# Kernel optimization log

Hardware: AMD Instinct MI355X
Metric: run time of the kernel (lower is better)

Reference implementation:

```python
import jax, jax.numpy as jnp
import numpy as np

B, S, E = 2, 4096, 640
H, D, G = 4, 256, 1      # n_heads, head_dim, n_kv_groups
WINDOW = 512
SCALING = 256.0 ** -0.5  # query_pre_attn_scalar ** -0.5
EPS = 1e-6


def rmsnorm(x, scale):
    # Gemma variant: weight = 1 + scale, computed in fp32 over last dim
    xf = x.astype(jnp.float32)
    var = jnp.mean(xf * xf, axis=-1, keepdims=True)
    return (xf * jax.lax.rsqrt(var + EPS) * (1.0 + scale.astype(jnp.float32))).astype(x.dtype)


def apply_rope(x, cos, sin):
    # x: [B, h, S, D]; cos/sin: [S, D]
    half = x.shape[-1] // 2
    x1, x2 = x[..., :half], x[..., half:]
    rotated = jnp.concatenate([-x2, x1], axis=-1)
    return (x * cos[None, None] + rotated * sin[None, None]).astype(x.dtype)


def setup_inputs() -> dict:
    key = jax.random.key(0)
    ks = jax.random.split(key, 6)
    x = jax.random.normal(ks[0], (B, S, E), dtype=jnp.float32)
    # weights (torch Linear weight.T layout: [in, out])
    Wq = jax.random.normal(ks[1], (E, H * D), dtype=jnp.float32) * 0.02
    Wk = jax.random.normal(ks[2], (E, G * D), dtype=jnp.float32) * 0.02
    Wv = jax.random.normal(ks[3], (E, G * D), dtype=jnp.float32) * 0.02
    Wo = jax.random.normal(ks[4], (H * D, E), dtype=jnp.float32) * 0.02
    q_scale = jnp.zeros((D,), dtype=jnp.float32)
    k_scale = jnp.zeros((D,), dtype=jnp.float32)
    # RoPE tables (theta = rope_local_base = 10000 for sliding layers)
    inv_freq = 1.0 / (10000.0 ** (jnp.arange(0, D, 2, dtype=jnp.float32) / D))
    angles = jnp.arange(S, dtype=jnp.float32)[:, None] * inv_freq[None, :]
    angles = jnp.concatenate([angles, angles], axis=1)  # [S, D]
    cos, sin = jnp.cos(angles), jnp.sin(angles)
    # causal + sliding-window mask; True = masked out
    i = jnp.arange(S)[:, None]
    j = jnp.arange(S)[None, :]
    mask = (j > i) | ((i - j) >= WINDOW)
    return {"x": x, "mask": mask, "cos": cos, "sin": sin,
            "Wq": Wq, "Wk": Wk, "Wv": Wv, "Wo": Wo,
            "q_scale": q_scale, "k_scale": k_scale}


def reference(x, mask, cos, sin, Wq, Wk, Wv, Wo, q_scale, k_scale):
    b, s, _ = x.shape
    q = (x @ Wq).reshape(b, s, H, D).transpose(0, 2, 1, 3)  # [B,H,S,D]
    k = (x @ Wk).reshape(b, s, G, D).transpose(0, 2, 1, 3)  # [B,G,S,D]
    v = (x @ Wv).reshape(b, s, G, D).transpose(0, 2, 1, 3)  # [B,G,S,D]
    q = rmsnorm(q, q_scale)
    k = rmsnorm(k, k_scale)
    q = apply_rope(q, cos, sin)
    k = apply_rope(k, cos, sin)
    # GQA: K/V have G=1 heads; broadcasting replaces repeat_interleave
    scores = (q * SCALING) @ jnp.swapaxes(k, -1, -2)  # [B,H,S,S]
    scores = jnp.where(mask[None, None], -jnp.inf, scores)
    attn = jax.nn.softmax(scores, axis=-1)
    out = attn @ v                                     # [B,H,S,D]
    out = out.transpose(0, 2, 1, 3).reshape(b, s, H * D)
    return out @ Wo
```

## Files before the change

kernel.cpp:

```cpp
#include <hip/hip_runtime.h>
#include <hip/hip_bf16.h>
#include <stdint.h>

#define BB 2
#define SS 4096
#define EE 640
#define HH 4
#define DD 256
#define WIN 512

typedef __attribute__((ext_vector_type(8))) short bv8;
typedef __attribute__((ext_vector_type(4))) float fv4;
typedef __attribute__((ext_vector_type(16))) float fv16;

__device__ __forceinline__ unsigned short f2b(float f) {
  union { float f; unsigned u; } a; a.f = f;
  unsigned r = a.u + 0x7fffu + ((a.u >> 16) & 1u);
  return (unsigned short)(r >> 16);
}
__device__ __forceinline__ float b2f(unsigned short s) {
  union { unsigned u; float f; } a; a.u = ((unsigned)s) << 16;
  return a.f;
}
__device__ __forceinline__ unsigned pk2(float lo, float hi_) {
  return (unsigned)f2b(lo) | ((unsigned)f2b(hi_) << 16);
}

typedef const __attribute__((address_space(1))) unsigned int* as1u;
typedef __attribute__((address_space(3))) unsigned int* as3u;
__device__ __forceinline__ void gld16(const unsigned short* g, unsigned short* l) {
  __builtin_amdgcn_global_load_lds((as1u)(const void*)g, (as3u)(void*)l, 16, 0, 0);
}

__global__ __launch_bounds__(256) void k_cast_bf16(const float* __restrict__ src,
                                                   unsigned short* __restrict__ dst, int n4) {
  int i = blockIdx.x * 256 + threadIdx.x;
  if (i >= n4) return;
  fv4 v = ((const fv4*)src)[i];
  ushort4 o; o.x = f2b(v.x); o.y = f2b(v.y); o.z = f2b(v.z); o.w = f2b(v.w);
  ((ushort4*)dst)[i] = o;
}

__global__ __launch_bounds__(256) void k_wtrans(const float* __restrict__ Wq,
    const float* __restrict__ Wk, const float* __restrict__ Wv,
    const float* __restrict__ Wo, const float* __restrict__ cosp,
    const float* __restrict__ sinp, unsigned short* __restrict__ wqkv,
    unsigned short* __restrict__ wo, float* __restrict__ ctab) {
  const int z = blockIdx.z, bx = blockIdx.x, by = blockIdx.y;
  const int t = threadIdx.x;
  if (z == 4) {
    const int bb = bx * 32 + by;
    const int s = bb * 4 + (t >> 6);
#pragma unroll
    for (int k = 0; k < 4; ++k) {
      int c = (t & 63) * 4 + k;
      int lr = c >> 4, wn2 = (c >> 3) & 1, j = c & 7;
      int d = wn2 * 64 + (j & 3) * 16 + lr;
      float v = (j < 4) ? cosp[(size_t)s * 256 + d] : sinp[(size_t)s * 256 + d];
      ctab[(size_t)s * 256 + c] = v;
    }
    return;
  }
  __shared__ float tile[32][33];
  const float* src; unsigned short* dst; int ss, ds;
  if (z == 0)      { if (bx >= 20 || by >= 32) return; src = Wq; dst = wqkv;              ss = 1024; ds = 640; }
  else if (z == 1) { if (bx >= 20 || by >= 8)  return; src = Wk; dst = wqkv + 1024 * 640; ss = 256;  ds = 640; }
  else if (z == 2) { if (bx >= 20 || by >= 8)  return; src = Wv; dst = wqkv + 1280 * 640; ss = 256;  ds = 640; }
  else             { if (bx >= 32 || by >= 20) return; src = Wo; dst = wo;                ss = 640;  ds = 1024; }
  int r0 = bx * 32, c0 = by * 32;
  int rr = t >> 3, cc = (t & 7) * 4;
  fv4 x = *(const fv4*)(src + (size_t)(r0 + rr) * ss + c0 + cc);
#pragma unroll
  for (int i = 0; i < 4; ++i) tile[cc + i][rr] = x[i];
  __syncthreads();
  ushort4 o;
  o.x = f2b(tile[rr][cc + 0]); o.y = f2b(tile[rr][cc + 1]);
  o.z = f2b(tile[rr][cc + 2]); o.w = f2b(tile[rr][cc + 3]);
  *(ushort4*)(dst + (size_t)(c0 + rr) * ds + r0 + cc) = o;
}

__global__ __launch_bounds__(256) void k_gemm_qkv(const unsigned short* __restrict__ A,
    const unsigned short* __restrict__ Bt, const float* __restrict__ ctab,
    const float* __restrict__ qsc, const float* __restrict__ ksc,
    unsigned short* __restrict__ qo, unsigned short* __restrict__ ko,
    unsigned short* __restrict__ vt) {
  __shared__ __align__(16) char shl[40960];
  unsigned short* la = (unsigned short*)shl;
  unsigned short* lb = (unsigned short*)(shl + 8192);
  const int K = EE;
  const int bid = blockIdx.x;
  const int gidx = (bid & 7) * 96 + (bid >> 3);
  const int mt = gidx / 6, nt = gidx % 6;
  const int m0 = mt * 64, n0 = nt * 256;
  const int tid = threadIdx.x, lane = tid & 63, wave = tid >> 6;
  const int g = lane >> 4, lr = lane & 15;
  const int wm = (wave >> 1) * 32, wn2 = wave & 1;
  fv4 acc[2][8] = {};
  const unsigned short* ga0 = A + (size_t)(m0 + (tid >> 2)) * K + (tid & 3) * 8;
  const unsigned short* gb0 = Bt + (size_t)(n0 + (tid >> 2)) * K + (tid & 3) * 8;
  auto stage = [&](int k0, int pp) {
    gld16(ga0 + k0, la + pp * 2048 + wave * 512);
#pragma unroll
    for (int c = 0; c < 4; ++c)
      gld16(gb0 + (size_t)(c * 64) * K + k0, lb + pp * 8192 + (c * 64 + wave * 16) * 32);
  };
  stage(0, 0);
  const int NIT = K >> 5;
  for (int it = 0; it < NIT; ++it) {
    const int p = it & 1;
    if (it > 0) __builtin_amdgcn_s_barrier();
    if (it + 1 < NIT) {
      stage((it + 1) * 32, p ^ 1);
      asm volatile("s_waitcnt vmcnt(5)" ::: "memory");
    } else {
      asm volatile("s_waitcnt vmcnt(0)" ::: "memory");
    }
    __builtin_amdgcn_sched_barrier(0);
    __builtin_amdgcn_s_barrier();
    bv8 af[2], bf[8];
#pragma unroll
    for (int mi = 0; mi < 2; ++mi)
      af[mi] = *(const bv8*)(la + p * 2048 + (wm + mi * 16 + lr) * 32 + g * 8);
#pragma unroll
    for (int ni = 0; ni < 8; ++ni) {
      int coln = wn2 * 64 + (ni & 3) * 16 + (ni >> 2) * 128 + lr;
      bf[ni] = *(const bv8*)(lb + p * 8192 + coln * 32 + g * 8);
    }
    __builtin_amdgcn_s_setprio(1);
#pragma unroll
    for (int mi = 0; mi < 2; ++mi)
#pragma unroll
      for (int ni = 0; ni < 8; ++ni)
        acc[mi][ni] = __builtin_amdgcn_mfma_f32_16x16x32_bf16(af[mi], bf[ni], acc[mi][ni], 0, 0, 0);
    __builtin_amdgcn_s_setprio(0);
  }
  __syncthreads();
  if (nt < 5) {
    float* rsum = (float*)(shl + 36864);
    float part[2][4];
#pragma unroll
    for (int mi = 0; mi < 2; ++mi)
#pragma unroll
      for (int r = 0; r < 4; ++r) {
        float ss2 = 0.f;
#pragma unroll
        for (int ni = 0; ni < 8; ++ni) ss2 += acc[mi][ni][r] * acc[mi][ni][r];
        part[mi][r] = ss2;
      }
#pragma unroll
    for (int off = 1; off < 16; off <<= 1)
#pragma unroll
      for (int mi = 0; mi < 2; ++mi)
#pragma unroll
        for (int r = 0; r < 4; ++r) part[mi][r] += __shfl_xor(part[mi][r], off, 64);
    if (lr == 0) {
#pragma unroll
      for (int mi = 0; mi < 2; ++mi)
#pragma unroll
        for (int r = 0; r < 4; ++r)
          rsum[(wm + mi * 16 + g * 4 + r) * 2 + wn2] = part[mi][r];
    }
    __syncthreads();
    const float* scp = (nt < 4) ? qsc : ksc;
    const float mult = (nt < 4) ? (0.0625f * 1.44269504f) : 1.0f;
    float scl[8];
#pragma unroll
    for (int ni = 0; ni < 8; ++ni) {
      int d = wn2 * 64 + (ni & 3) * 16 + (ni >> 2) * 128 + lr;
      scl[ni] = 1.0f + scp[d];
    }
#pragma unroll
    for (int mi = 0; mi < 2; ++mi)
#pragma unroll
      for (int r = 0; r < 4; ++r) {
        int row = wm + mi * 16 + g * 4 + r;
        int mabs = m0 + row;
        int bb = mabs >> 12, s = mabs & 4095;
        float tot = rsum[row * 2 + 0] + rsum[row * 2 + 1];
        float rs = rsqrtf(tot * (1.0f / 256.0f) + 1e-6f);
        fv4 c4 = *(const fv4*)(ctab + (size_t)s * 256 + lr * 16 + wn2 * 8);
        fv4 s4 = *(const fv4*)(ctab + (size_t)s * 256 + lr * 16 + wn2 * 8 + 4);
        unsigned short* dst = (nt < 4)
            ? qo + ((size_t)(bb * HH + nt) * SS + s) * 256
            : ko + ((size_t)bb * SS + s) * 256;
#pragma unroll
        for (int j = 0; j < 4; ++j) {
          float nlo = acc[mi][j][r] * rs * scl[j];
          float nhi = acc[mi][j + 4][r] * rs * scl[j + 4];
          float olo = (nlo * c4[j] - nhi * s4[j]) * mult;
          float ohi = (nhi * c4[j] + nlo * s4[j]) * mult;
          int dlo = wn2 * 64 + j * 16 + lr;
          dst[dlo] = f2b(olo);
          dst[dlo + 128] = f2b(ohi);
        }
      }
  } else {
    unsigned short* vcol = (unsigned short*)shl;
#pragma unroll
    for (int mi = 0; mi < 2; ++mi)
#pragma unroll
      for (int ni = 0; ni < 8; ++ni) {
        int col = wn2 * 64 + (ni & 3) * 16 + (ni >> 2) * 128 + lr;
        int row0 = wm + mi * 16 + g * 4;
        uint2 u;
        u.x = pk2(acc[mi][ni][0], acc[mi][ni][1]);
        u.y = pk2(acc[mi][ni][2], acc[mi][ni][3]);
        *(uint2*)(vcol + col * 72 + row0) = u;
      }
    __syncthreads();
    const int d = tid;
    const int bb0 = m0 >> 12, s0 = m0 & 4095;
    unsigned short* dst = vt + ((size_t)bb0 * 256 + d) * SS + s0;
#pragma unroll
    for (int c8 = 0; c8 < 8; ++c8) {
      bv8 v = *(const bv8*)(vcol + d * 72 + c8 * 8);
      *(bv8*)(dst + c8 * 8) = v;
    }
  }
}

template <bool OUT_BF16, int BN>
__global__ __launch_bounds__(256) void k_gemm(const unsigned short* __restrict__ A,
    const unsigned short* __restrict__ Bt, void* __restrict__ Cp,
    int M, int N, int K, int nt_n) {
  __shared__ unsigned short la[2][128 * 32];
  __shared__ unsigned short lb[2][BN * 32];
  const int bid = blockIdx.x;
  const int gidx = (bid & 7) * (gridDim.x >> 3) + (bid >> 3);
  const int m0 = (gidx / nt_n) * 128, n0 = (gidx % nt_n) * BN;
  const int tid = threadIdx.x, lane = tid & 63, wave = tid >> 6;
  const int g = lane >> 4, lr = lane & 15;
  constexpr int MI = (BN == 128) ? 4 : 2;
  const int wm = (BN == 128) ? (wave >> 1) * 64 : wave * 32;
  const int wn = (BN == 128) ? (wave & 1) * 64 : 0;
  fv4 acc[MI][4] = {};
  const int srow = wave * 32 + (lane >> 2);
  const int sch = (lane & 3) * 8;
  const unsigned short* ga0 = A + (size_t)(m0 + srow) * K + sch;
  const int srowb = (BN == 128) ? srow : (wave * 16 + (lane >> 2));
  const unsigned short* gb0 = Bt + (size_t)(n0 + srowb) * K + sch;
  const int NIT = K >> 5;
  auto stage = [&](int k0, int pp) {
    unsigned short* lad = la[pp] + wave * 1024;
    unsigned short* lbd = lb[pp] + ((BN == 128) ? wave * 1024 : wave * 512);
    gld16(ga0 + k0, lad);
    gld16(ga0 + (size_t)16 * K + k0, lad + 512);
    gld16(gb0 + k0, lbd);
    if constexpr (BN == 128) gld16(gb0 + (size_t)16 * K + k0, lbd + 512);
  };
  stage(0, 0);
  for (int it = 0; it < NIT; ++it) {
    const int p = it & 1;
    if (it > 0) __builtin_amdgcn_s_barrier();
    if (it + 1 < NIT) {
      stage((it + 1) * 32, p ^ 1);
      if constexpr (BN == 128)
        asm volatile("s_waitcnt vmcnt(4)" ::: "memory");
      else
        asm volatile("s_waitcnt vmcnt(3)" ::: "memory");
    } else {
      asm volatile("s_waitcnt vmcnt(0)" ::: "memory");
    }
    __builtin_amdgcn_sched_barrier(0);
    __builtin_amdgcn_s_barrier();
    bv8 af[MI], bf[4];
#pragma unroll
    for (int mi = 0; mi < MI; ++mi)
      af[mi] = *(const bv8*)(la[p] + (wm + mi * 16 + lr) * 32 + g * 8);
#pragma unroll
    for (int ni = 0; ni < 4; ++ni)
      bf[ni] = *(const bv8*)(lb[p] + (wn + ni * 16 + lr) * 32 + g * 8);
    __builtin_amdgcn_s_setprio(1);
#pragma unroll
    for (int mi = 0; mi < MI; ++mi)
#pragma unroll
      for (int ni = 0; ni < 4; ++ni)
        acc[mi][ni] = __builtin_amdgcn_mfma_f32_16x16x32_bf16(af[mi], bf[ni], acc[mi][ni], 0, 0, 0);
    __builtin_amdgcn_s_setprio(0);
  }
#pragma unroll
  for (int mi = 0; mi < MI; ++mi) {
#pragma unroll
    for (int r = 0; r < 4; ++r) {
      size_t row = (size_t)(m0 + wm + mi * 16 + g * 4 + r);
#pragma unroll
      for (int ni = 0; ni < 4; ++ni) {
        int col = n0 + wn + ni * 16 + lr;
        float val = acc[mi][ni][r];
        if constexpr (OUT_BF16)
          ((unsigned short*)Cp)[row * N + col] = f2b(val);
        else
          ((float*)Cp)[row * N + col] = val;
      }
    }
  }
}

__global__ __launch_bounds__(512, 2) void k_attn(const unsigned short* __restrict__ q,
    const unsigned short* __restrict__ kg, const unsigned short* __restrict__ vtg,
    unsigned short* __restrict__ att) {
  __shared__ __align__(16) char ldsbuf[133120];
  __shared__ float lsb[4][32];
  unsigned short* kt = (unsigned short*)ldsbuf;
  unsigned short* vl = (unsigned short*)ldsbuf + 32768;
  const int bid = blockIdx.x;
  const int gidx = (bid & 7) * 32 + (bid >> 3);
  const int b = gidx >> 7;
  const int i0 = (gidx & 127) * 32;
  const int tid = threadIdx.x, wave = tid >> 6, lane = tid & 63;
  const int h = wave >> 1, ks = wave & 1;
  const int hi = lane >> 5, l31 = lane & 31;
  bv8 qf[16];
  {
    const unsigned short* qp = q + ((size_t)(b * HH + h) * SS + i0 + l31) * 256;
#pragma unroll
    for (int m = 0; m < 16; ++m) qf[m] = *(const bv8*)(qp + m * 16 + hi * 8);
  }
  fv16 po[8] = {};
  float lsp = 0.f;
  const int t0 = (i0 >= WIN) ? ((i0 - WIN + 1) >> 6) : 0;
  const int t1 = i0 >> 6;
  const unsigned short* kb = kg + (size_t)b * SS * 256;
  const unsigned short* vb = vtg + (size_t)b * 256 * SS;
  auto stageK = [&](int t, int pp) {
    const unsigned short* kbase = kb + (size_t)t * 64 * 256;
    unsigned short* dst = kt + pp * 16384;
#pragma unroll
    for (int c = 0; c < 4; ++c) {
      int slot = c * 512 + tid;
      int row = slot >> 5, s = slot & 31;
      gld16(kbase + (size_t)row * 256 + ((s ^ (row & 7)) * 8),
            dst + (c * 512 + wave * 64) * 8);
    }
  };
  auto stageV = [&](int t, int pp) {
    const unsigned short* vbase = vb + (size_t)t * 64;
    unsigned short* dst = vl + pp * 16384;
#pragma unroll
    for (int c = 0; c < 4; ++c) {
      int slot = c * 512 + tid;
      int d_ = slot >> 3, s = slot & 7;
      gld16(vbase + (size_t)d_ * SS + ((s ^ (d_ & 7)) * 8),
            dst + (c * 512 + wave * 64) * 8);
    }
  };
  stageK(t0, 0); stageV(t0, 0);
  int p = 0;
  const int krow = ks * 32 + l31;
  const int krx = krow & 7;
  const int vrx = l31 & 7;
  const float FSUB = 16.5f * 1.44269504f;
  for (int t = t0; t <= t1; ++t) {
    __syncthreads();
    if (t < t1) { stageK(t + 1, p ^ 1); stageV(t + 1, p ^ 1); }
    fv16 sa = {};
    const unsigned short* ktp = kt + p * 16384 + krow * 256;
    __builtin_amdgcn_s_setprio(1);
#pragma unroll
    for (int m = 0; m < 16; ++m) {
      bv8 kf = *(const bv8*)(ktp + (((m * 2 + hi) ^ krx) * 8));
      sa = __builtin_amdgcn_mfma_f32_32x32x16_bf16(kf, qf[m], sa, 0, 0, 0);
    }
    __builtin_amdgcn_s_setprio(0);
    const int kb0 = t * 64 + ks * 32;
    const bool nm = (kb0 + 31 > i0) || (i0 + 31 - kb0 >= WIN);
    if (nm) {
      const int qa = i0 + l31;
#pragma unroll
      for (int r = 0; r < 16; ++r) {
        int j = kb0 + (r & 3) + 8 * (r >> 2) + 4 * hi;
        if (j > qa || qa - j >= WIN) sa[r] = -1e30f;
      }
    }
    unsigned a[8];
#pragma unroll
    for (int i = 0; i < 8; ++i) {
      float e0 = exp2f(sa[2 * i] - FSUB);
      float e1 = exp2f(sa[2 * i + 1] - FSUB);
      lsp += e0 + e1;
      a[i] = pk2(e0, e1);
    }
    const unsigned short* vlp = vl + p * 16384;
    __builtin_amdgcn_s_setprio(1);
#pragma unroll
    for (int m2 = 0; m2 < 2; ++m2) {
      auto r02 = __builtin_amdgcn_permlane32_swap(a[m2 * 4 + 0], a[m2 * 4 + 2], false, false);
      auto r13 = __builtin_amdgcn_permlane32_swap(a[m2 * 4 + 1], a[m2 * 4 + 3], false, false);
      union { unsigned u[4]; bv8 v; } pf;
      pf.u[0] = r02[0]; pf.u[1] = r13[0]; pf.u[2] = r02[1]; pf.u[3] = r13[1];
      const int slot = (ks * 4 + m2 * 2 + hi) ^ vrx;
#pragma unroll
      for (int ds_ = 0; ds_ < 8; ++ds_) {
        bv8 vf = *(const bv8*)(vlp + (ds_ * 32 + l31) * 64 + slot * 8);
        po[ds_] = __builtin_amdgcn_mfma_f32_32x32x16_bf16(vf, pf.v, po[ds_], 0, 0, 0);
      }
    }
    __builtin_amdgcn_s_setprio(0);
    p ^= 1;
  }
  float lsfull = lsp + __shfl_xor(lsp, 32, 64);
  __syncthreads();
  float* cb = (float*)ldsbuf;
  if (ks == 1) {
#pragma unroll
    for (int ds_ = 0; ds_ < 8; ++ds_)
#pragma unroll
      for (int j = 0; j < 4; ++j) {
        int d0 = ds_ * 32 + 8 * j + 4 * hi;
        fv4 v4; v4[0] = po[ds_][4 * j]; v4[1] = po[ds_][4 * j + 1];
        v4[2] = po[ds_][4 * j + 2]; v4[3] = po[ds_][4 * j + 3];
        *(fv4*)(cb + (h * 32 + l31) * 260 + d0) = v4;
      }
    if (lane < 32) lsb[h][lane] = lsfull;
  }
  __syncthreads();
  if (ks == 0) {
    float total = lsfull + lsb[h][l31];
    float inv = 1.0f / total;
    unsigned short* op = att + ((size_t)b * SS + i0 + l31) * 1024 + h * 256;
#pragma unroll
    for (int ds_ = 0; ds_ < 8; ++ds_)
#pragma unroll
      for (int j = 0; j < 4; ++j) {
        int d0 = ds_ * 32 + 8 * j + 4 * hi;
        fv4 v4 = *(const fv4*)(cb + (h * 32 + l31) * 260 + d0);
        ushort4 o;
        o.x = f2b((po[ds_][4 * j] + v4[0]) * inv);
        o.y = f2b((po[ds_][4 * j + 1] + v4[1]) * inv);
        o.z = f2b((po[ds_][4 * j + 2] + v4[2]) * inv);
        o.w = f2b((po[ds_][4 * j + 3] + v4[3]) * inv);
        *(ushort4*)(op + d0) = o;
      }
  }
}

extern "C" void kernel_launch(void* const* d_in, const int* in_sizes, int n_in,
                              void* d_out, int out_size, void* d_ws, size_t ws_size,
                              hipStream_t stream) {
  const float* x    = (const float*)d_in[0];
  const float* cosp = (const float*)d_in[2];
  const float* sinp = (const float*)d_in[3];
  const float* Wq   = (const float*)d_in[4];
  const float* Wk   = (const float*)d_in[5];
  const float* Wv   = (const float*)d_in[6];
  const float* Wo   = (const float*)d_in[7];
  const float* qsc  = (const float*)d_in[8];
  const float* ksc  = (const float*)d_in[9];
  float* out = (float*)d_out;
  char* ws = (char*)d_ws;

  unsigned short* xb   = (unsigned short*)(ws);
  unsigned short* wqkv = (unsigned short*)(ws + 10485760);
  unsigned short* wo   = (unsigned short*)(ws + 12451840);
  float*          ctab = (float*)(ws + 13762560);
  unsigned short* qb   = (unsigned short*)(ws + 38928384);
  unsigned short* kbuf = (unsigned short*)(ws + 55705600);
  unsigned short* vt   = (unsigned short*)(ws + 59899904);
  unsigned short* attb = (unsigned short*)(ws + 64094208);

  k_cast_bf16<<<5120, 256, 0, stream>>>(x, xb, 1310720);
  k_wtrans<<<dim3(32, 32, 5), 256, 0, stream>>>(Wq, Wk, Wv, Wo, cosp, sinp, wqkv, wo, ctab);
  k_gemm_qkv<<<768, 256, 0, stream>>>(xb, wqkv, ctab, qsc, ksc, qb, kbuf, vt);
  k_attn<<<256, 512, 0, stream>>>(qb, kbuf, vt, attb);
  k_gemm<false, 64><<<640, 256, 0, stream>>>(attb, wo, out, 8192, 640, 1024, 10);
}
```

Baseline: 112.1 us.

## Fold x bf16 cast into weight-prep launch and shrink output GEMM tiles

The separate x-to-bf16 cast kernel is merged into the weight transpose kernel as an extra grid z-slice, which removes one kernel launch. The output projection GEMM is specialised into a 64x64-tile kernel with 1280 blocks instead of 128x64 tiles with 640 blocks, so more CUs get work for the 8192x640 output. The cost is more redundant A/B tile loads per output element and fewer MFMAs per LDS fetch.

```diff
diff --git a/kernel.cpp b/kernel.cpp
--- a/kernel.cpp
+++ b/kernel.cpp
@@ -32,22 +32,25 @@
   __builtin_amdgcn_global_load_lds((as1u)(const void*)g, (as3u)(void*)l, 16, 0, 0);
 }
 
-__global__ __launch_bounds__(256) void k_cast_bf16(const float* __restrict__ src,
-                                                   unsigned short* __restrict__ dst, int n4) {
-  int i = blockIdx.x * 256 + threadIdx.x;
-  if (i >= n4) return;
-  fv4 v = ((const fv4*)src)[i];
-  ushort4 o; o.x = f2b(v.x); o.y = f2b(v.y); o.z = f2b(v.z); o.w = f2b(v.w);
-  ((ushort4*)dst)[i] = o;
-}
-
 __global__ __launch_bounds__(256) void k_wtrans(const float* __restrict__ Wq,
     const float* __restrict__ Wk, const float* __restrict__ Wv,
     const float* __restrict__ Wo, const float* __restrict__ cosp,
-    const float* __restrict__ sinp, unsigned short* __restrict__ wqkv,
-    unsigned short* __restrict__ wo, float* __restrict__ ctab) {
+    const float* __restrict__ sinp, const float* __restrict__ x,
+    unsigned short* __restrict__ wqkv, unsigned short* __restrict__ wo,
+    float* __restrict__ ctab, unsigned short* __restrict__ xb) {
   const int z = blockIdx.z, bx = blockIdx.x, by = blockIdx.y;
   const int t = threadIdx.x;
+  if (z == 5) {
+    const int bb = bx * 32 + by;
+#pragma unroll
+    for (int u = 0; u < 5; ++u) {
+      int i = bb * 1280 + u * 256 + t;
+      fv4 v = ((const fv4*)x)[i];
+      ushort4 o; o.x = f2b(v.x); o.y = f2b(v.y); o.z = f2b(v.z); o.w = f2b(v.w);
+      ((ushort4*)xb)[i] = o;
+    }
+    return;
+  }
   if (z == 4) {
     const int bb = bx * 32 + by;
     const int s = bb * 4 + (t >> 6);
@@ -69,9 +72,9 @@
   else             { if (bx >= 32 || by >= 20) return; src = Wo; dst = wo;                ss = 640;  ds = 1024; }
   int r0 = bx * 32, c0 = by * 32;
   int rr = t >> 3, cc = (t & 7) * 4;
-  fv4 x = *(const fv4*)(src + (size_t)(r0 + rr) * ss + c0 + cc);
-#pragma unroll
-  for (int i = 0; i < 4; ++i) tile[cc + i][rr] = x[i];
+  fv4 xv = *(const fv4*)(src + (size_t)(r0 + rr) * ss + c0 + cc);
+#pragma unroll
+  for (int i = 0; i < 4; ++i) tile[cc + i][rr] = xv[i];
   __syncthreads();
   ushort4 o;
   o.x = f2b(tile[rr][cc + 0]); o.y = f2b(tile[rr][cc + 1]);
@@ -219,80 +222,55 @@
   }
 }
 
-template <bool OUT_BF16, int BN>
-__global__ __launch_bounds__(256) void k_gemm(const unsigned short* __restrict__ A,
-    const unsigned short* __restrict__ Bt, void* __restrict__ Cp,
-    int M, int N, int K, int nt_n) {
-  __shared__ unsigned short la[2][128 * 32];
-  __shared__ unsigned short lb[2][BN * 32];
+__global__ __launch_bounds__(256) void k_gout(const unsigned short* __restrict__ A,
+    const unsigned short* __restrict__ Bt, float* __restrict__ Cp) {
+  __shared__ unsigned short la[2][64 * 32];
+  __shared__ unsigned short lb[2][64 * 32];
+  const int K = 1024, N = 640;
   const int bid = blockIdx.x;
-  const int gidx = (bid & 7) * (gridDim.x >> 3) + (bid >> 3);
-  const int m0 = (gidx / nt_n) * 128, n0 = (gidx % nt_n) * BN;
+  const int gidx = (bid & 7) * 160 + (bid >> 3);
+  const int m0 = (gidx / 10) * 64, n0 = (gidx % 10) * 64;
   const int tid = threadIdx.x, lane = tid & 63, wave = tid >> 6;
   const int g = lane >> 4, lr = lane & 15;
-  constexpr int MI = (BN == 128) ? 4 : 2;
-  const int wm = (BN == 128) ? (wave >> 1) * 64 : wave * 32;
-  const int wn = (BN == 128) ? (wave & 1) * 64 : 0;
-  fv4 acc[MI][4] = {};
-  const int srow = wave * 32 + (lane >> 2);
+  fv4 acc[4] = {};
+  const int srow = wave * 16 + (lane >> 2);
   const int sch = (lane & 3) * 8;
   const unsigned short* ga0 = A + (size_t)(m0 + srow) * K + sch;
-  const int srowb = (BN == 128) ? srow : (wave * 16 + (lane >> 2));
-  const unsigned short* gb0 = Bt + (size_t)(n0 + srowb) * K + sch;
-  const int NIT = K >> 5;
+  const unsigned short* gb0 = Bt + (size_t)(n0 + srow) * K + sch;
   auto stage = [&](int k0, int pp) {
-    unsigned short* lad = la[pp] + wave * 1024;
-    unsigned short* lbd = lb[pp] + ((BN == 128) ? wave * 1024 : wave * 512);
-    gld16(ga0 + k0, lad);
-    gld16(ga0 + (size_t)16 * K + k0, lad + 512);
-    gld16(gb0 + k0, lbd);
-    if constexpr (BN == 128) gld16(gb0 + (size_t)16 * K + k0, lbd + 512);
+    gld16(ga0 + k0, la[pp] + wave * 512);
+    gld16(gb0 + k0, lb[pp] + wave * 512);
   };
   stage(0, 0);
+  const int NIT = 32;
   for (int it = 0; it < NIT; ++it) {
     const int p = it & 1;
     if (it > 0) __builtin_amdgcn_s_barrier();
     if (it + 1 < NIT) {
       stage((it + 1) * 32, p ^ 1);
-      if constexpr (BN == 128)
-        asm volatile("s_waitcnt vmcnt(4)" ::: "memory");
-      else
-        asm volatile("s_waitcnt vmcnt(3)" ::: "memory");
+      asm volatile("s_waitcnt vmcnt(2)" ::: "memory");
     } else {
       asm volatile("s_waitcnt vmcnt(0)" ::: "memory");
     }
     __builtin_amdgcn_sched_barrier(0);
     __builtin_amdgcn_s_barrier();
-    bv8 af[MI], bf[4];
-#pragma unroll
-    for (int mi = 0; mi < MI; ++mi)
-      af[mi] = *(const bv8*)(la[p] + (wm + mi * 16 + lr) * 32 + g * 8);
+    bv8 af = *(const bv8*)(la[p] + (wave * 16 + lr) * 32 + g * 8);
+    bv8 bf[4];
 #pragma unroll
     for (int ni = 0; ni < 4; ++ni)
-      bf[ni] = *(const bv8*)(lb[p] + (wn + ni * 16 + lr) * 32 + g * 8);
+      bf[ni] = *(const bv8*)(lb[p] + (ni * 16 + lr) * 32 + g * 8);
     __builtin_amdgcn_s_setprio(1);
 #pragma unroll
-    for (int mi = 0; mi < MI; ++mi)
-#pragma unroll
-      for (int ni = 0; ni < 4; ++ni)
-        acc[mi][ni] = __builtin_amdgcn_mfma_f32_16x16x32_bf16(af[mi], bf[ni], acc[mi][ni], 0, 0, 0);
+    for (int ni = 0; ni < 4; ++ni)
+      acc[ni] = __builtin_amdgcn_mfma_f32_16x16x32_bf16(af, bf[ni], acc[ni], 0, 0, 0);
     __builtin_amdgcn_s_setprio(0);
   }
 #pragma unroll
-  for (int mi = 0; mi < MI; ++mi) {
-#pragma unroll
-    for (int r = 0; r < 4; ++r) {
-      size_t row = (size_t)(m0 + wm + mi * 16 + g * 4 + r);
-#pragma unroll
-      for (int ni = 0; ni < 4; ++ni) {
-        int col = n0 + wn + ni * 16 + lr;
-        float val = acc[mi][ni][r];
-        if constexpr (OUT_BF16)
-          ((unsigned short*)Cp)[row * N + col] = f2b(val);
-        else
-          ((float*)Cp)[row * N + col] = val;
-      }
-    }
+  for (int r = 0; r < 4; ++r) {
+    size_t row = (size_t)(m0 + wave * 16 + g * 4 + r);
+#pragma unroll
+    for (int ni = 0; ni < 4; ++ni)
+      Cp[row * N + n0 + ni * 16 + lr] = acc[ni][r];
   }
 }
 
@@ -458,9 +436,9 @@
   unsigned short* vt   = (unsigned short*)(ws + 59899904);
   unsigned short* attb = (unsigned short*)(ws + 64094208);
 
-  k_cast_bf16<<<5120, 256, 0, stream>>>(x, xb, 1310720);
-  k_wtrans<<<dim3(32, 32, 5), 256, 0, stream>>>(Wq, Wk, Wv, Wo, cosp, sinp, wqkv, wo, ctab);
+  k_wtrans<<<dim3(32, 32, 6), 256, 0, stream>>>(Wq, Wk, Wv, Wo, cosp, sinp, x,
+                                                wqkv, wo, ctab, xb);
   k_gemm_qkv<<<768, 256, 0, stream>>>(xb, wqkv, ctab, qsc, ksc, qb, kbuf, vt);
   k_attn<<<256, 512, 0, stream>>>(qb, kbuf, vt, attb);
-  k_gemm<false, 64><<<640, 256, 0, stream>>>(attb, wo, out, 8192, 640, 1024, 10);
-}
+  k_gout<<<1280, 256, 0, stream>>>(attb, wo, out);
+}
```

New measurement: 113.5 us. About the same (+1.2%).
